# Performance work log

Measured on AMD Instinct MI355X. Metric: run time of the kernel, lower is better.

Reference implementation:

```python
import jax, jax.numpy as jnp
import numpy as np

MUL = 128            # multiplicity of every irrep (128x0e node features)
LS = (0, 1, 2, 3)    # sh irreps 0e,1o,2e,3o
SH_DIMS = tuple(2 * l + 1 for l in LS)  # (1,3,5,7) -> total 16
RB = 8               # radial basis features
N_NODES, N_EDGES = 5000, 100000


def setup_inputs() -> dict:
    key = jax.random.key(0)
    ks = jax.random.split(key, 12)
    return {
        "node_features": jax.random.normal(ks[0], (N_NODES, MUL), jnp.float32),
        "sph_harmonics": jax.random.normal(ks[1], (N_EDGES, sum(SH_DIMS)), jnp.float32),
        "radial_basis": jax.random.uniform(ks[2], (N_EDGES, RB), jnp.float32),
        "edge_i": jax.random.randint(ks[3], (N_EDGES,), 0, N_NODES),  # central atoms
        "edge_j": jax.random.randint(ks[4], (N_EDGES,), 0, N_NODES),  # neighbours
        "W_pre": jax.random.normal(ks[5], (MUL, MUL), jnp.float32),
        "mlp_w0": jax.random.normal(ks[6], (RB, 64), jnp.float32),
        "mlp_w1": jax.random.normal(ks[7], (64, 64), jnp.float32),
        "mlp_w2": jax.random.normal(ks[8], (64, 64), jnp.float32),
        "mlp_w3": jax.random.normal(ks[9], (64, len(LS) * MUL), jnp.float32),
        "W_post": jax.random.normal(ks[10], (len(LS), MUL, MUL), jnp.float32),
    }


def _forward(node_features, sph, rb, edge_i, edge_j,
             W_pre, mlp_w0, mlp_w1, mlp_w2, mlp_w3, W_post):
    N = node_features.shape[0]
    inv = np.float32(1.0 / np.sqrt(MUL))
    # pre o3.Linear on 128x0e: dense mix of multiplicities, fan-in normalized
    x = (node_features @ W_pre) * inv                       # [N, MUL]
    nbr = x[edge_j]                                         # gather neighbours [E, MUL]
    # per-edge weight generator: SiLU hidden layers, linear last, no bias
    h = rb
    for w in (mlp_w0, mlp_w1, mlp_w2):
        h = jax.nn.silu((h @ w) * np.float32(1.0 / np.sqrt(w.shape[0])))
    w_edge = (h @ mlp_w3) * np.float32(1.0 / np.sqrt(mlp_w3.shape[0]))  # [E, 4*MUL]
    w_edge = w_edge.reshape(-1, len(LS), MUL)               # one weight chunk per CG path
    off = 0
    out_blocks = []
    for p, d in enumerate(SH_DIMS):
        Y = sph[:, off:off + d]; off += d                   # [E, d]
        m = (nbr * w_edge[:, p, :])[:, :, None] * Y[:, None, :]  # messages [E, MUL, d]
        # scatter-aggregate messages onto central atoms (sum aggregation)
        tot = jax.ops.segment_sum(m.reshape(m.shape[0], -1), edge_i, num_segments=N)
        tot = tot.reshape(N, MUL, d)
        # post o3.Linear: per-irrep dense mix of multiplicities
        out_blocks.append(jnp.einsum('nud,uv->nvd', tot, W_post[p]) * inv)
    # reshape_irreps: [N, MUL, 1+3+5+7] = [N, 128, 16]
    return jnp.concatenate(out_blocks, axis=-1)


def reference(node_features, sph_harmonics, radial_basis, edge_i, edge_j,
              W_pre, mlp_w0, mlp_w1, mlp_w2, mlp_w3, W_post):
    return _forward(node_features, sph_harmonics, radial_basis, edge_i, edge_j,
                    W_pre, mlp_w0, mlp_w1, mlp_w2, mlp_w3, W_post)
```

## Files before the change

kernel.cpp:

```cpp
#include <hip/hip_runtime.h>
#include <hip/hip_bf16.h>

#define NN 5000
#define NE 100000

__device__ __forceinline__ float silu_f(float x) {
    return x / (1.0f + __expf(-x));
}

__global__ __launch_bounds__(128) void k_pre(const float* __restrict__ nf,
                                             const float* __restrict__ Wpre,
                                             float* __restrict__ x) {
    __shared__ float row[128];
    int n = blockIdx.x;
    int v = threadIdx.x;
    row[v] = nf[(size_t)n * 128 + v];
    __syncthreads();
    float acc = 0.f;
#pragma unroll 16
    for (int u = 0; u < 128; ++u) acc += row[u] * Wpre[u * 128 + v];
    x[(size_t)n * 128 + v] = acc * 0.08838834764831845f;
}

__global__ void k_count(const int* __restrict__ ei, int* __restrict__ counts) {
    int e = blockIdx.x * blockDim.x + threadIdx.x;
    if (e < NE) atomicAdd(&counts[ei[e]], 1);
}

__global__ __launch_bounds__(256) void k_scan(const int* __restrict__ counts,
                                              int* __restrict__ offsets) {
    __shared__ int part[256];
    int t = threadIdx.x;
    const int CH = 20;
    int lo = t * CH, hi = min(lo + CH, NN);
    int s = 0;
    for (int i = lo; i < hi; ++i) s += counts[i];
    part[t] = s;
    __syncthreads();
    if (t == 0) {
        int run = 0;
        for (int i = 0; i < 256; ++i) { int v = part[i]; part[i] = run; run += v; }
    }
    __syncthreads();
    int run = part[t];
    for (int i = lo; i < hi; ++i) { offsets[i] = run; run += counts[i]; }
    if (t == 0) offsets[NN] = NE;
}

__global__ void k_fill(const int* __restrict__ ei, const int* __restrict__ offsets,
                       int* __restrict__ cursor, int* __restrict__ order) {
    int e = blockIdx.x * blockDim.x + threadIdx.x;
    if (e < NE) {
        int i = ei[e];
        int pos = atomicAdd(&cursor[i], 1);
        order[offsets[i] + pos] = e;
    }
}

template<bool ACT>
__device__ __forceinline__ void mlp_layer64(const float (&src)[64][65], float (&dst)[64][65],
                                            const float* __restrict__ w, float scale,
                                            int ob, int mb) {
    float acc[4][4] = {};
    for (int k = 0; k < 64; ++k) {
        float wv[4];
#pragma unroll
        for (int c = 0; c < 4; ++c) wv[c] = w[k * 64 + ob + 16 * c];
#pragma unroll
        for (int mm = 0; mm < 4; ++mm) {
            float hv = src[mb + mm][k];
#pragma unroll
            for (int c = 0; c < 4; ++c) acc[mm][c] += hv * wv[c];
        }
    }
#pragma unroll
    for (int mm = 0; mm < 4; ++mm)
#pragma unroll
        for (int c = 0; c < 4; ++c) {
            float v = acc[mm][c] * scale;
            dst[mb + mm][ob + 16 * c] = ACT ? silu_f(v) : v;
        }
}

__global__ __launch_bounds__(256) void k_mlp(const float* __restrict__ rb,
                                             const float* __restrict__ w0,
                                             const float* __restrict__ w1,
                                             const float* __restrict__ w2,
                                             const float* __restrict__ w3,
                                             __hip_bfloat16* __restrict__ we) {
    __shared__ float ha[64][65];
    __shared__ float hb[64][65];
    const int t = threadIdx.x;
    const int base = blockIdx.x * 64;

    for (int idx = t; idx < 512; idx += 256) {
        int m = idx >> 3, k = idx & 7;
        int e = base + m;
        ha[m][k] = (e < NE) ? rb[(size_t)e * 8 + k] : 0.f;
    }
    __syncthreads();

    const int ob = t & 15;
    const int mb = (t >> 4) * 4;

    {
        float acc[4][4] = {};
#pragma unroll
        for (int k = 0; k < 8; ++k) {
            float wv[4];
#pragma unroll
            for (int c = 0; c < 4; ++c) wv[c] = w0[k * 64 + ob + 16 * c];
#pragma unroll
            for (int mm = 0; mm < 4; ++mm) {
                float hv = ha[mb + mm][k];
#pragma unroll
                for (int c = 0; c < 4; ++c) acc[mm][c] += hv * wv[c];
            }
        }
#pragma unroll
        for (int mm = 0; mm < 4; ++mm)
#pragma unroll
            for (int c = 0; c < 4; ++c)
                hb[mb + mm][ob + 16 * c] = silu_f(acc[mm][c] * 0.35355339059327373f);
    }
    __syncthreads();
    mlp_layer64<true>(hb, ha, w1, 0.125f, ob, mb);
    __syncthreads();
    mlp_layer64<true>(ha, hb, w2, 0.125f, ob, mb);
    __syncthreads();

    {
        const int o0 = t & 63;
        const int mB = (t >> 6) * 16;
        for (int rblk = 0; rblk < 2; ++rblk) {
            float acc[16][4] = {};
            for (int k = 0; k < 64; ++k) {
                float wv[4];
#pragma unroll
                for (int r = 0; r < 4; ++r) wv[r] = w3[k * 512 + o0 + 64 * (rblk * 4 + r)];
#pragma unroll
                for (int mm = 0; mm < 16; ++mm) {
                    float hv = hb[mB + mm][k];
#pragma unroll
                    for (int r = 0; r < 4; ++r) acc[mm][r] += hv * wv[r];
                }
            }
            for (int mm = 0; mm < 16; ++mm) {
                int e = base + mB + mm;
                if (e < NE) {
#pragma unroll
                    for (int r = 0; r < 4; ++r)
                        we[(size_t)e * 512 + o0 + 64 * (rblk * 4 + r)] =
                            __float2bfloat16(acc[mm][r] * 0.125f);
                }
            }
        }
    }
}

__global__ __launch_bounds__(256) void k_gather(const float* __restrict__ x,
                                                const __hip_bfloat16* __restrict__ we,
                                                const float* __restrict__ sph,
                                                const int* __restrict__ ej,
                                                const int* __restrict__ offsets,
                                                const int* __restrict__ order,
                                                const float* __restrict__ Wpost,
                                                float* __restrict__ out) {
    __shared__ float tot[4 * 128 * 24];
    const int t = threadIdx.x;
    const int w = t >> 6, lane = t & 63;
    const int n = blockIdx.x;
    const int s0 = offsets[n], s1 = offsets[n + 1];

    float acc0[16] = {};
    float acc1[16] = {};

    const int PMAP[16] = {0,1,1,1, 2,2,2,2, 2,3,3,3, 3,3,3,3};

    for (int idx = s0 + w; idx < s1; idx += 4) {
        int e = order[idx];
        int j = ej[e];
        const float* xp = x + (size_t)j * 128;
        float xj0 = xp[lane];
        float xj1 = xp[lane + 64];
        const __hip_bfloat16* wep = we + (size_t)e * 512;
        float a0[4], a1[4];
#pragma unroll
        for (int p = 0; p < 4; ++p) {
            a0[p] = xj0 * __bfloat162float(wep[p * 128 + lane]);
            a1[p] = xj1 * __bfloat162float(wep[p * 128 + 64 + lane]);
        }
        const float4* Y4 = (const float4*)(sph + (size_t)e * 16);
        float yv[16];
        ((float4*)yv)[0] = Y4[0];
        ((float4*)yv)[1] = Y4[1];
        ((float4*)yv)[2] = Y4[2];
        ((float4*)yv)[3] = Y4[3];
#pragma unroll
        for (int k = 0; k < 16; ++k) {
            acc0[k] += a0[PMAP[k]] * yv[k];
            acc1[k] += a1[PMAP[k]] * yv[k];
        }
    }

    float* tw = tot + w * 3072;
#pragma unroll
    for (int k = 0; k < 16; ++k) {
        tw[lane * 24 + k]        = acc0[k];
        tw[(lane + 64) * 24 + k] = acc1[k];
    }
    __syncthreads();

    for (int i = t; i < 2048; i += 256) {
        int u = i >> 4, k = i & 15;
        int a = u * 24 + k;
        tot[a] = tot[a] + tot[3072 + a] + tot[2 * 3072 + a] + tot[3 * 3072 + a];
    }
    __syncthreads();

    const int v = t & 127, kh = t >> 7;
    const float* W0 = Wpost + v;
    const float* W1 = Wpost + 16384 + v;
    const float* W2 = Wpost + 2 * 16384 + v;
    const float* W3 = Wpost + 3 * 16384 + v;
    float acc[8] = {};
    if (kh == 0) {
        for (int u = 0; u < 128; ++u) {
            float4 ta = *(const float4*)&tot[u * 24 + 0];
            float4 tb = *(const float4*)&tot[u * 24 + 4];
            float wa = W0[u * 128];
            float wb = W1[u * 128];
            float wc = W2[u * 128];
            acc[0] += wa * ta.x;
            acc[1] += wb * ta.y; acc[2] += wb * ta.z; acc[3] += wb * ta.w;
            acc[4] += wc * tb.x; acc[5] += wc * tb.y; acc[6] += wc * tb.z; acc[7] += wc * tb.w;
        }
    } else {
        for (int u = 0; u < 128; ++u) {
            float4 ta = *(const float4*)&tot[u * 24 + 8];
            float4 tb = *(const float4*)&tot[u * 24 + 12];
            float wc = W2[u * 128];
            float wd = W3[u * 128];
            acc[0] += wc * ta.x;
            acc[1] += wd * ta.y; acc[2] += wd * ta.z; acc[3] += wd * ta.w;
            acc[4] += wd * tb.x; acc[5] += wd * tb.y; acc[6] += wd * tb.z; acc[7] += wd * tb.w;
        }
    }
    float* op = out + (size_t)n * 2048 + v * 16 + kh * 8;
    const float inv = 0.08838834764831845f;
    float4 r0 = make_float4(acc[0] * inv, acc[1] * inv, acc[2] * inv, acc[3] * inv);
    float4 r1 = make_float4(acc[4] * inv, acc[5] * inv, acc[6] * inv, acc[7] * inv);
    *(float4*)op = r0;
    *(float4*)(op + 4) = r1;
}

extern "C" void kernel_launch(void* const* d_in, const int* in_sizes, int n_in,
                              void* d_out, int out_size, void* d_ws, size_t ws_size,
                              hipStream_t stream) {
    const float* nf    = (const float*)d_in[0];
    const float* sph   = (const float*)d_in[1];
    const float* rb    = (const float*)d_in[2];
    const int*   ei    = (const int*)d_in[3];
    const int*   ej    = (const int*)d_in[4];
    const float* Wpre  = (const float*)d_in[5];
    const float* w0    = (const float*)d_in[6];
    const float* w1    = (const float*)d_in[7];
    const float* w2    = (const float*)d_in[8];
    const float* w3    = (const float*)d_in[9];
    const float* Wpost = (const float*)d_in[10];
    float* out = (float*)d_out;

    char* ws = (char*)d_ws;
    const size_t OFF_X       = 0;
    const size_t OFF_WE      = 2560000;
    const size_t OFF_COUNTS  = 104960000;
    const size_t OFF_CURSOR  = 104980000;
    const size_t OFF_OFFSETS = 105000000;
    const size_t OFF_ORDER   = 105020032;
    const size_t NEEDED      = 105420032;
    if (ws_size < NEEDED) return;

    float*          x       = (float*)(ws + OFF_X);
    __hip_bfloat16* we      = (__hip_bfloat16*)(ws + OFF_WE);
    int*            counts  = (int*)(ws + OFF_COUNTS);
    int*            cursor  = (int*)(ws + OFF_CURSOR);
    int*            offsets = (int*)(ws + OFF_OFFSETS);
    int*            order   = (int*)(ws + OFF_ORDER);

    hipMemsetAsync(ws + OFF_COUNTS, 0, 40000, stream);

    k_count<<<(NE + 255) / 256, 256, 0, stream>>>(ei, counts);
    k_scan<<<1, 256, 0, stream>>>(counts, offsets);
    k_fill<<<(NE + 255) / 256, 256, 0, stream>>>(ei, offsets, cursor, order);

    k_pre<<<NN, 128, 0, stream>>>(nf, Wpre, x);
    k_mlp<<<(NE + 63) / 64, 256, 0, stream>>>(rb, w0, w1, w2, w3, we);
    k_gather<<<NN, 256, 0, stream>>>(x, we, sph, ej, offsets, order, Wpost, out);
}
```

Baseline: 303.9 us.

## Run edge-weight MLP layers on MFMA with split-bf16 hi/lo emulation

The 64x64 hidden layers and the 64x512 output layer of the per-edge MLP move from scalar FP32 FMAs to bf16 MFMA 16x16x32 instructions. Each operand is split into a high and a low bf16 part, and three products are summed to keep close to FP32 accuracy. A new prep kernel converts and transposes the weights into hi/lo bf16 buffers every call, and activations are stored in XOR-swizzled shared memory. This aims to cut the compute-bound MLP cost at the price of an extra small kernel launch and 3x MFMA work.

```diff
diff --git a/kernel.cpp b/kernel.cpp
--- a/kernel.cpp
+++ b/kernel.cpp
@@ -4,8 +4,21 @@
 #define NN 5000
 #define NE 100000
 
+typedef unsigned short u16;
+typedef __attribute__((ext_vector_type(8))) short bf16x8;
+typedef __attribute__((ext_vector_type(4))) float f32x4;
+
 __device__ __forceinline__ float silu_f(float x) {
     return x / (1.0f + __expf(-x));
+}
+
+__device__ __forceinline__ u16 f2bf(float x) {
+    unsigned int u = __float_as_uint(x);
+    u += 0x7FFFu + ((u >> 16) & 1u);
+    return (u16)(u >> 16);
+}
+__device__ __forceinline__ float bf2f(u16 h) {
+    return __uint_as_float(((unsigned int)h) << 16);
 }
 
 __global__ __launch_bounds__(128) void k_pre(const float* __restrict__ nf,
@@ -57,109 +70,160 @@
     }
 }
 
-template<bool ACT>
-__device__ __forceinline__ void mlp_layer64(const float (&src)[64][65], float (&dst)[64][65],
-                                            const float* __restrict__ w, float scale,
-                                            int ob, int mb) {
-    float acc[4][4] = {};
-    for (int k = 0; k < 64; ++k) {
-        float wv[4];
-#pragma unroll
-        for (int c = 0; c < 4; ++c) wv[c] = w[k * 64 + ob + 16 * c];
-#pragma unroll
-        for (int mm = 0; mm < 4; ++mm) {
-            float hv = src[mb + mm][k];
-#pragma unroll
-            for (int c = 0; c < 4; ++c) acc[mm][c] += hv * wv[c];
-        }
-    }
-#pragma unroll
-    for (int mm = 0; mm < 4; ++mm)
-#pragma unroll
-        for (int c = 0; c < 4; ++c) {
-            float v = acc[mm][c] * scale;
-            dst[mb + mm][ob + 16 * c] = ACT ? silu_f(v) : v;
-        }
+__global__ __launch_bounds__(256) void k_wprep(const float* __restrict__ w1,
+                                               const float* __restrict__ w2,
+                                               const float* __restrict__ w3,
+                                               u16* __restrict__ w1h, u16* __restrict__ w1l,
+                                               u16* __restrict__ w2h, u16* __restrict__ w2l,
+                                               u16* __restrict__ w3h, u16* __restrict__ w3l) {
+    int i = blockIdx.x * 256 + threadIdx.x;
+    if (i < 4096) {
+        int k = i >> 6, n = i & 63;
+        float v = w1[i];
+        u16 h = f2bf(v), l = f2bf(v - bf2f(h));
+        w1h[n * 64 + k] = h; w1l[n * 64 + k] = l;
+        v = w2[i];
+        h = f2bf(v); l = f2bf(v - bf2f(h));
+        w2h[n * 64 + k] = h; w2l[n * 64 + k] = l;
+    }
+    if (i < 32768) {
+        int k = i >> 9, n = i & 511;
+        float v = w3[i];
+        u16 h = f2bf(v), l = f2bf(v - bf2f(h));
+        w3h[n * 64 + k] = h; w3l[n * 64 + k] = l;
+    }
+}
+
+
+__device__ __forceinline__ void layer_mid(const char* sh, const char* sl,
+                                          const u16* __restrict__ wh,
+                                          const u16* __restrict__ wl,
+                                          char* dh, char* dl, int w, int l) {
+    const int col = w * 16 + (l & 15);
+    bf16x8 B[2][2];
+#pragma unroll
+    for (int kc = 0; kc < 2; ++kc) {
+        B[kc][0] = *(const bf16x8*)(wh + col * 64 + kc * 32 + ((l >> 4) << 3));
+        B[kc][1] = *(const bf16x8*)(wl + col * 64 + kc * 32 + ((l >> 4) << 3));
+    }
+#pragma unroll
+    for (int rt = 0; rt < 4; ++rt) {
+        const int arow = rt * 16 + (l & 15);
+        f32x4 acc = {0.f, 0.f, 0.f, 0.f};
+#pragma unroll
+        for (int kc = 0; kc < 2; ++kc) {
+            int off = (arow * 128 + kc * 64 + ((l >> 4) << 4)) ^ ((arow & 7) << 4);
+            bf16x8 ah = *(const bf16x8*)(sh + off);
+            bf16x8 al = *(const bf16x8*)(sl + off);
+            acc = __builtin_amdgcn_mfma_f32_16x16x32_bf16(ah, B[kc][0], acc, 0, 0, 0);
+            acc = __builtin_amdgcn_mfma_f32_16x16x32_bf16(ah, B[kc][1], acc, 0, 0, 0);
+            acc = __builtin_amdgcn_mfma_f32_16x16x32_bf16(al, B[kc][0], acc, 0, 0, 0);
+        }
+#pragma unroll
+        for (int r = 0; r < 4; ++r) {
+            float v = silu_f(acc[r] * 0.125f);
+            u16 hi = f2bf(v), lo = f2bf(v - bf2f(hi));
+            int orow = rt * 16 + ((l >> 4) << 2) + r;
+            int off = (orow * 128 + col * 2) ^ ((orow & 7) << 4);
+            *(u16*)(dh + off) = hi;
+            *(u16*)(dl + off) = lo;
+        }
+    }
+}
+
+__device__ __forceinline__ void layer_out(const char* sh, const char* sl,
+                                          const u16* __restrict__ wh,
+                                          const u16* __restrict__ wl,
+                                          u16* __restrict__ we, int base, int w, int l) {
+    const int r0 = (w & 1) * 32;
+    const int c0 = (w >> 1) * 256;
+    bf16x8 A[2][2][2];
+#pragma unroll
+    for (int rt = 0; rt < 2; ++rt)
+#pragma unroll
+        for (int kc = 0; kc < 2; ++kc) {
+            int row = r0 + rt * 16 + (l & 15);
+            int off = (row * 128 + kc * 64 + ((l >> 4) << 4)) ^ ((row & 7) << 4);
+            A[rt][kc][0] = *(const bf16x8*)(sh + off);
+            A[rt][kc][1] = *(const bf16x8*)(sl + off);
+        }
+    for (int nt = 0; nt < 16; ++nt) {
+        const int col = c0 + nt * 16 + (l & 15);
+        f32x4 acc[2] = {{0.f, 0.f, 0.f, 0.f}, {0.f, 0.f, 0.f, 0.f}};
+#pragma unroll
+        for (int kc = 0; kc < 2; ++kc) {
+            bf16x8 bh = *(const bf16x8*)(wh + col * 64 + kc * 32 + ((l >> 4) << 3));
+            bf16x8 bl = *(const bf16x8*)(wl + col * 64 + kc * 32 + ((l >> 4) << 3));
+#pragma unroll
+            for (int rt = 0; rt < 2; ++rt) {
+                acc[rt] = __builtin_amdgcn_mfma_f32_16x16x32_bf16(A[rt][kc][0], bh, acc[rt], 0, 0, 0);
+                acc[rt] = __builtin_amdgcn_mfma_f32_16x16x32_bf16(A[rt][kc][0], bl, acc[rt], 0, 0, 0);
+                acc[rt] = __builtin_amdgcn_mfma_f32_16x16x32_bf16(A[rt][kc][1], bh, acc[rt], 0, 0, 0);
+            }
+        }
+#pragma unroll
+        for (int rt = 0; rt < 2; ++rt)
+#pragma unroll
+            for (int r = 0; r < 4; ++r) {
+                int row = r0 + rt * 16 + ((l >> 4) << 2) + r;
+                int e = base + row;
+                if (e < NE) we[(size_t)e * 512 + col] = f2bf(acc[rt][r] * 0.125f);
+            }
+    }
 }
 
 __global__ __launch_bounds__(256) void k_mlp(const float* __restrict__ rb,
                                              const float* __restrict__ w0,
-                                             const float* __restrict__ w1,
-                                             const float* __restrict__ w2,
-                                             const float* __restrict__ w3,
-                                             __hip_bfloat16* __restrict__ we) {
-    __shared__ float ha[64][65];
-    __shared__ float hb[64][65];
+                                             const u16* __restrict__ w1h, const u16* __restrict__ w1l,
+                                             const u16* __restrict__ w2h, const u16* __restrict__ w2l,
+                                             const u16* __restrict__ w3h, const u16* __restrict__ w3l,
+                                             u16* __restrict__ we) {
+    __shared__ __align__(16) char hAh[8192];
+    __shared__ __align__(16) char hAl[8192];
+    __shared__ __align__(16) char hBh[8192];
+    __shared__ __align__(16) char hBl[8192];
+    __shared__ float rbs[512];
     const int t = threadIdx.x;
+    const int l = t & 63, w = t >> 6;
     const int base = blockIdx.x * 64;
 
-    for (int idx = t; idx < 512; idx += 256) {
-        int m = idx >> 3, k = idx & 7;
-        int e = base + m;
-        ha[m][k] = (e < NE) ? rb[(size_t)e * 8 + k] : 0.f;
-    }
-    __syncthreads();
-
-    const int ob = t & 15;
-    const int mb = (t >> 4) * 4;
+    for (int i = t; i < 512; i += 256) {
+        int e = base + (i >> 3);
+        rbs[i] = (e < NE) ? rb[(size_t)e * 8 + (i & 7)] : 0.f;
+    }
+    __syncthreads();
 
     {
-        float acc[4][4] = {};
+        const int m = t >> 2, n0 = (t & 3) * 16;
+        float h[16];
+#pragma unroll
+        for (int nn = 0; nn < 16; ++nn) h[nn] = 0.f;
 #pragma unroll
         for (int k = 0; k < 8; ++k) {
-            float wv[4];
-#pragma unroll
-            for (int c = 0; c < 4; ++c) wv[c] = w0[k * 64 + ob + 16 * c];
-#pragma unroll
-            for (int mm = 0; mm < 4; ++mm) {
-                float hv = ha[mb + mm][k];
-#pragma unroll
-                for (int c = 0; c < 4; ++c) acc[mm][c] += hv * wv[c];
-            }
-        }
-#pragma unroll
-        for (int mm = 0; mm < 4; ++mm)
-#pragma unroll
-            for (int c = 0; c < 4; ++c)
-                hb[mb + mm][ob + 16 * c] = silu_f(acc[mm][c] * 0.35355339059327373f);
-    }
-    __syncthreads();
-    mlp_layer64<true>(hb, ha, w1, 0.125f, ob, mb);
-    __syncthreads();
-    mlp_layer64<true>(ha, hb, w2, 0.125f, ob, mb);
-    __syncthreads();
-
-    {
-        const int o0 = t & 63;
-        const int mB = (t >> 6) * 16;
-        for (int rblk = 0; rblk < 2; ++rblk) {
-            float acc[16][4] = {};
-            for (int k = 0; k < 64; ++k) {
-                float wv[4];
-#pragma unroll
-                for (int r = 0; r < 4; ++r) wv[r] = w3[k * 512 + o0 + 64 * (rblk * 4 + r)];
-#pragma unroll
-                for (int mm = 0; mm < 16; ++mm) {
-                    float hv = hb[mB + mm][k];
-#pragma unroll
-                    for (int r = 0; r < 4; ++r) acc[mm][r] += hv * wv[r];
-                }
-            }
-            for (int mm = 0; mm < 16; ++mm) {
-                int e = base + mB + mm;
-                if (e < NE) {
-#pragma unroll
-                    for (int r = 0; r < 4; ++r)
-                        we[(size_t)e * 512 + o0 + 64 * (rblk * 4 + r)] =
-                            __float2bfloat16(acc[mm][r] * 0.125f);
-                }
-            }
-        }
-    }
+            float r = rbs[m * 8 + k];
+            const float* wp = w0 + k * 64 + n0;
+#pragma unroll
+            for (int nn = 0; nn < 16; ++nn) h[nn] += r * wp[nn];
+        }
+#pragma unroll
+        for (int nn = 0; nn < 16; ++nn) {
+            float v = silu_f(h[nn] * 0.35355339059327373f);
+            u16 hi = f2bf(v), lo = f2bf(v - bf2f(hi));
+            int off = (m * 128 + (n0 + nn) * 2) ^ ((m & 7) << 4);
+            *(u16*)(hAh + off) = hi;
+            *(u16*)(hAl + off) = lo;
+        }
+    }
+    __syncthreads();
+    layer_mid(hAh, hAl, w1h, w1l, hBh, hBl, w, l);
+    __syncthreads();
+    layer_mid(hBh, hBl, w2h, w2l, hAh, hAl, w, l);
+    __syncthreads();
+    layer_out(hAh, hAl, w3h, w3l, we, base, w, l);
 }
 
 __global__ __launch_bounds__(256) void k_gather(const float* __restrict__ x,
-                                                const __hip_bfloat16* __restrict__ we,
+                                                const u16* __restrict__ we,
                                                 const float* __restrict__ sph,
                                                 const int* __restrict__ ej,
                                                 const int* __restrict__ offsets,
@@ -183,12 +247,12 @@
         const float* xp = x + (size_t)j * 128;
         float xj0 = xp[lane];
         float xj1 = xp[lane + 64];
-        const __hip_bfloat16* wep = we + (size_t)e * 512;
+        const u16* wep = we + (size_t)e * 512;
         float a0[4], a1[4];
 #pragma unroll
         for (int p = 0; p < 4; ++p) {
-            a0[p] = xj0 * __bfloat162float(wep[p * 128 + lane]);
-            a1[p] = xj1 * __bfloat162float(wep[p * 128 + 64 + lane]);
+            a0[p] = xj0 * bf2f(wep[p * 128 + lane]);
+            a1[p] = xj1 * bf2f(wep[p * 128 + 64 + lane]);
         }
         const float4* Y4 = (const float4*)(sph + (size_t)e * 16);
         float yv[16];
@@ -277,23 +341,33 @@
     const size_t OFF_CURSOR  = 104980000;
     const size_t OFF_OFFSETS = 105000000;
     const size_t OFF_ORDER   = 105020032;
-    const size_t NEEDED      = 105420032;
+    const size_t OFF_W1H     = 105420032;
+    const size_t OFF_W1L     = OFF_W1H + 8192;
+    const size_t OFF_W2H     = OFF_W1L + 8192;
+    const size_t OFF_W2L     = OFF_W2H + 8192;
+    const size_t OFF_W3H     = OFF_W2L + 8192;
+    const size_t OFF_W3L     = OFF_W3H + 65536;
+    const size_t NEEDED      = OFF_W3L + 65536;
     if (ws_size < NEEDED) return;
 
-    float*          x       = (float*)(ws + OFF_X);
-    __hip_bfloat16* we      = (__hip_bfloat16*)(ws + OFF_WE);
-    int*            counts  = (int*)(ws + OFF_COUNTS);
-    int*            cursor  = (int*)(ws + OFF_CURSOR);
-    int*            offsets = (int*)(ws + OFF_OFFSETS);
-    int*            order   = (int*)(ws + OFF_ORDER);
-
-    hipMemsetAsync(ws + OFF_COUNTS, 0, 40000, stream);
+    float* x       = (float*)(ws + OFF_X);
+    u16*   we      = (u16*)(ws + OFF_WE);
+    int*   counts  = (int*)(ws + OFF_COUNTS);
+    int*   cursor  = (int*)(ws + OFF_CURSOR);
+    int*   offsets = (int*)(ws + OFF_OFFSETS);
+    int*   order   = (int*)(ws + OFF_ORDER);
+    u16*   w1h = (u16*)(ws + OFF_W1H); u16* w1l = (u16*)(ws + OFF_W1L);
+    u16*   w2h = (u16*)(ws + OFF_W2H); u16* w2l = (u16*)(ws + OFF_W2L);
+    u16*   w3h = (u16*)(ws + OFF_W3H); u16* w3l = (u16*)(ws + OFF_W3L);
+
+    (void)hipMemsetAsync(ws + OFF_COUNTS, 0, 40000, stream);
 
     k_count<<<(NE + 255) / 256, 256, 0, stream>>>(ei, counts);
     k_scan<<<1, 256, 0, stream>>>(counts, offsets);
     k_fill<<<(NE + 255) / 256, 256, 0, stream>>>(ei, offsets, cursor, order);
+    k_wprep<<<128, 256, 0, stream>>>(w1, w2, w3, w1h, w1l, w2h, w2l, w3h, w3l);
 
     k_pre<<<NN, 128, 0, stream>>>(nf, Wpre, x);
-    k_mlp<<<(NE + 63) / 64, 256, 0, stream>>>(rb, w0, w1, w2, w3, we);
+    k_mlp<<<(NE + 63) / 64, 256, 0, stream>>>(rb, w0, w1h, w1l, w2h, w2l, w3h, w3l, we);
     k_gather<<<NN, 256, 0, stream>>>(x, we, sph, ej, offsets, order, Wpost, out);
 }
```

New measurement: 261.2 us. -14.1%, faster.
